# Performance work log

Hardware: AMD Instinct MI355X
Metric: run time of the kernel (lower is better)

## Reference

```python
import jax, jax.numpy as jnp
import numpy as np

G = 16          # spline grid_size
NT = 32         # num_tiles
NS = 2          # num_states
SD = 8          # state_dim
MAXLEN = 2048.0 # max_seq_len
SPREAD = 2.0    # position_spread
LN_EPS = 1e-5


def cubic_bspline(t):
    t = jnp.abs(t)
    r1 = 2.0 / 3.0 - t * t + 0.5 * t ** 3
    r2 = (1.0 / 6.0) * (2.0 - t) ** 3
    return jnp.where(t < 1.0, r1, jnp.where(t < 2.0, r2, jnp.zeros_like(t)))


def ternary(x):
    return jnp.where(x > 0.3, 1.0, jnp.where(x < -0.3, -1.0, 0.0)).astype(x.dtype)


def setup_inputs() -> dict:
    key = jax.random.key(0)
    ks = jax.random.split(key, 14)
    B, T, D = 4, 2048, 1024
    H = D // 4
    x = jax.random.normal(ks[0], (B, T, D), jnp.float32)
    positions = jnp.broadcast_to(jnp.arange(T, dtype=jnp.float32), (B, T))
    states = jax.random.randint(ks[1], (B, T), 0, NS)
    ln_gamma = jnp.ones((D,), jnp.float32)
    ln_beta = jnp.zeros((D,), jnp.float32)
    W1 = jax.random.normal(ks[2], (D, H), jnp.float32) * (1.0 / np.sqrt(D))
    b1 = jnp.zeros((H,), jnp.float32)
    W2 = jax.random.normal(ks[3], (H, 2), jnp.float32) * (1.0 / np.sqrt(H))
    b2 = jnp.zeros((2,), jnp.float32)
    spline_coeffs = jax.random.normal(ks[4], (NT, G, G, 3), jnp.float32) * 0.5
    spline_scales = jnp.ones((NT,), jnp.float32)
    directions = jax.random.normal(ks[5], (NT, D), jnp.float32) * 0.02
    state_signatures = jax.random.normal(ks[6], (NT, SD), jnp.float32) * 0.1
    state_emb = jax.random.normal(ks[7], (NS, SD), jnp.float32)
    state_mod = jnp.ones((NS, NT), jnp.float32)
    output_scale = jnp.ones((1,), jnp.float32) * 0.1
    return dict(x=x, positions=positions, states=states, ln_gamma=ln_gamma,
                ln_beta=ln_beta, W1=W1, b1=b1, W2=W2, b2=b2,
                spline_coeffs=spline_coeffs, spline_scales=spline_scales,
                directions=directions, state_signatures=state_signatures,
                state_emb=state_emb, state_mod=state_mod, output_scale=output_scale)


def reference(x, positions, states, ln_gamma, ln_beta, W1, b1, W2, b2,
              spline_coeffs, spline_scales, directions, state_signatures,
              state_emb, state_mod, output_scale):
    B, T, D = x.shape
    xf = x.reshape(-1, D)                               # [N, D]
    mu = jnp.mean(xf, axis=-1, keepdims=True)
    var = jnp.mean((xf - mu) ** 2, axis=-1, keepdims=True)
    xn = (xf - mu) / jnp.sqrt(var + LN_EPS) * ln_gamma + ln_beta

    # --- three-way routing ---
    sigs = jnp.sign(directions)                         # ternary signatures [NT, D]
    content = xn @ sigs.T                               # [N, NT]
    pos = positions.reshape(-1)
    pn = pos / MAXLEN * NT
    centers = jnp.arange(NT, dtype=xn.dtype)
    spatial = cubic_bspline((pn[:, None] - centers[None, :]) / SPREAD)  # [N, NT]
    st = states.reshape(-1)
    sv = state_emb[st]                                  # [N, SD]
    temporal = jax.nn.sigmoid(sv @ state_signatures.T)  # [N, NT]
    combined = content * spatial * temporal
    probs = jax.nn.softmax(combined * 5.0, axis=-1)
    tile_idx = jnp.argmax(combined, axis=-1)            # [N]
    tile_weights = jnp.take_along_axis(probs, tile_idx[:, None], axis=1)[:, 0]

    # --- compress to 2D spline coordinates ---
    h = jax.nn.gelu(xn @ W1 + b1, approximate=False)
    comp = jnp.tanh(h @ W2 + b2)                        # [N, 2]
    a, b = comp[:, 0], comp[:, 1]

    # --- ternary 2D spline per winning tile (vectorized dispatch) ---
    idx_a = jnp.clip(((a + 1.0) / 2.0 * G).astype(jnp.int32), 0, G - 1)
    idx_b = jnp.clip(((b + 1.0) / 2.0 * G).astype(jnp.int32), 0, G - 1)
    q = spline_coeffs + jax.lax.stop_gradient(ternary(spline_coeffs) - spline_coeffs)
    cell = q[tile_idx, idx_a, idx_b]                    # [N, 3]
    cs = 2.0 / G
    la = (a + 1.0 - idx_a.astype(a.dtype) * cs) / cs
    lb = (b + 1.0 - idx_b.astype(b.dtype) * cs) / cs
    scale = (cell[:, 0] + cell[:, 1] * la + cell[:, 2] * lb) * spline_scales[tile_idx]
    smod = state_mod[st, tile_idx]
    contrib = (scale * smod)[:, None] * directions[tile_idx]  # [N, D]

    out = x + contrib.reshape(B, T, D) * output_scale   # residual, eval (no dropout)
    return out
```

## Files before the change

kernel.cpp:

```cpp
#include <hip/hip_runtime.h>
#include <math.h>

#define NROWS 8192
#define DD    1024
#define HH    256
#define NTT   32
#define NCOLS 288

typedef __attribute__((ext_vector_type(8))) __bf16 bf16x8;
typedef __attribute__((ext_vector_type(4))) float f32x4;

static __device__ __forceinline__ unsigned short f2bf(float f) {
    unsigned int u = __float_as_uint(f);
    unsigned int r = (u + 0x7fffu + ((u >> 16) & 1u)) >> 16;
    return (unsigned short)r;
}

static __device__ __forceinline__ float sgnf(float x) {
    return x > 0.0f ? 1.0f : (x < 0.0f ? -1.0f : 0.0f);
}

static __device__ __forceinline__ float ternf(float x) {
    return x > 0.3f ? 1.0f : (x < -0.3f ? -1.0f : 0.0f);
}

static __device__ __forceinline__ float bspline(float u) {
    float t = fabsf(u);
    if (t < 1.0f) return 0.66666666666666663f - t * t + 0.5f * t * t * t;
    if (t < 2.0f) { float w = 2.0f - t; return 0.16666666666666666f * w * w * w; }
    return 0.0f;
}

__global__ __launch_bounds__(256) void k_prep_ln(const float* __restrict__ W1,
                                                 const float* __restrict__ dirs,
                                                 const float* __restrict__ gamma,
                                                 const float* __restrict__ beta,
                                                 const float* __restrict__ x,
                                                 unsigned short* __restrict__ WT,
                                                 unsigned short* __restrict__ XN) {
    int bid = blockIdx.x;
    int tid = threadIdx.x;
    if (bid < 256) {
        __shared__ float tile[32][33];
        int ktile = bid & 31;
        int ntile = bid >> 5;
        int tx = tid & 31;
        int ty = tid >> 5;
#pragma unroll
        for (int i = 0; i < 4; ++i) {
            int k = ktile * 32 + ty + i * 8;
            int n = ntile * 32 + tx;
            tile[ty + i * 8][tx] = W1[(size_t)k * HH + n];
        }
        __syncthreads();
#pragma unroll
        for (int i = 0; i < 4; ++i) {
            int n = ntile * 32 + ty + i * 8;
            int k = ktile * 32 + tx;
            WT[(size_t)n * DD + k] = f2bf(tile[tx][ty + i * 8]);
        }
    } else if (bid < 288) {
        int r = bid - 256;
        float4 v = ((const float4*)(dirs + (size_t)r * DD))[tid];
        ushort4 o;
        o.x = f2bf(sgnf(v.x)); o.y = f2bf(sgnf(v.y));
        o.z = f2bf(sgnf(v.z)); o.w = f2bf(sgnf(v.w));
        ((ushort4*)(WT + (size_t)(HH + r) * DD))[tid] = o;
    } else {
        int row = bid - 288;
        const float4* xr = (const float4*)(x + (size_t)row * DD);
        float4 v = xr[tid];
        float s  = v.x + v.y + v.z + v.w;
        float sq = v.x * v.x + v.y * v.y + v.z * v.z + v.w * v.w;
#pragma unroll
        for (int off = 32; off; off >>= 1) {
            s  += __shfl_xor(s, off);
            sq += __shfl_xor(sq, off);
        }
        __shared__ float red[8];
        int wid = tid >> 6, lane = tid & 63;
        if (lane == 0) { red[wid] = s; red[wid + 4] = sq; }
        __syncthreads();
        s  = red[0] + red[1] + red[2] + red[3];
        sq = red[4] + red[5] + red[6] + red[7];
        float mu   = s * (1.0f / DD);
        float var  = sq * (1.0f / DD) - mu * mu;
        float rstd = rsqrtf(var + 1e-5f);
        float4 gm = ((const float4*)gamma)[tid];
        float4 bt = ((const float4*)beta)[tid];
        ushort4 o;
        o.x = f2bf((v.x - mu) * rstd * gm.x + bt.x);
        o.y = f2bf((v.y - mu) * rstd * gm.y + bt.y);
        o.z = f2bf((v.z - mu) * rstd * gm.z + bt.z);
        o.w = f2bf((v.w - mu) * rstd * gm.w + bt.w);
        ((ushort4*)(XN + (size_t)row * DD))[tid] = o;
    }
}

__global__ __launch_bounds__(256) void k_gemm(const unsigned short* __restrict__ XN,
                                              const unsigned short* __restrict__ WT,
                                              float* __restrict__ HP) {
    __shared__ short Al[2][32 * 64];
    __shared__ short Bl[2][96 * 64];
    int tid = threadIdx.x;
    int bid = blockIdx.x;
    int swz = (bid & 7) * 96 + (bid >> 3);
    int colblk = swz % 3;
    int rowblk = swz / 3;
    int row0  = rowblk * 32;
    int ncol0 = colblk * 96;
    int lane = tid & 63;
    int wid  = tid >> 6;
    int wm = wid >> 1, wn = wid & 1;
    int l15 = lane & 15, l4 = lane >> 4;

    f32x4 acc[3];
#pragma unroll
    for (int j = 0; j < 3; ++j) acc[j] = (f32x4){0.f, 0.f, 0.f, 0.f};

#define STAGE(kt, buf)                                                           \
    {                                                                            \
                           \
        {                                                                        \
            int r = tid >> 3, g = tid & 7;                                       \
            const unsigned short* srcA =                                         \
                XN + (size_t)(row0 + r) * DD + (kt) * 64 + ((g * 8) ^ ((r & 7) << 3)); \
            __builtin_amdgcn_global_load_lds(                                    \
                (const __attribute__((address_space(1))) void*)(const void*)srcA,\
                (__attribute__((address_space(3))) void*)(void*)(Al[buf] + tid * 8), \
                16, 0, 0);                                                       \
        }                                                                        \
                                            \
        _Pragma("unroll")                                                        \
        for (int ci = 0; ci < 3; ++ci) {                                         \
            int li = ci * 256 + tid;                                             \
            int r  = li >> 3;                                                    \
            int g  = li & 7;                                                     \
            const unsigned short* src =                                          \
                WT + (size_t)(ncol0 + r) * DD + (kt) * 64 + ((g * 8) ^ ((r & 7) << 3)); \
            __builtin_amdgcn_global_load_lds(                                    \
                (const __attribute__((address_space(1))) void*)(const void*)src, \
                (__attribute__((address_space(3))) void*)(void*)(Bl[buf] + li * 8), \
                16, 0, 0);                                                       \
        }                                                                        \
    }

#define COMPUTE(buf)                                                             \
    _Pragma("unroll")                                                            \
    for (int ks = 0; ks < 2; ++ks) {                                             \
        int ra = wm * 16 + l15;                                                  \
        int ca = (ks * 64 + l4 * 16) ^ ((ra & 7) << 4);                          \
        bf16x8 av = *(const bf16x8*)((const char*)Al[buf] + ra * 128 + ca);      \
        bf16x8 bv[3];                                                            \
        _Pragma("unroll")                                                        \
        for (int nf = 0; nf < 3; ++nf) {                                         \
            int rb = wn * 48 + nf * 16 + l15;                                    \
            int cb = (ks * 64 + l4 * 16) ^ ((rb & 7) << 4);                      \
            bv[nf] = *(const bf16x8*)((const char*)Bl[buf] + rb * 128 + cb);     \
        }                                                                        \
        _Pragma("unroll")                                                        \
        for (int nf = 0; nf < 3; ++nf)                                           \
            acc[nf] = __builtin_amdgcn_mfma_f32_16x16x32_bf16(av, bv[nf], acc[nf], 0, 0, 0); \
    }

    STAGE(0, 0);
    __syncthreads();
    for (int kt = 0; kt < 16; ++kt) {
        if (kt < 15) STAGE(kt + 1, (kt + 1) & 1);
        COMPUTE(kt & 1);
        __syncthreads();
    }
#undef STAGE
#undef COMPUTE

#pragma unroll
    for (int nf = 0; nf < 3; ++nf) {
        int colg = ncol0 + wn * 48 + nf * 16 + l15;
        int rl0 = wm * 16 + l4 * 4;
#pragma unroll
        for (int i = 0; i < 4; ++i) {
            HP[(size_t)(row0 + rl0 + i) * NCOLS + colg] = acc[nf][i];
        }
    }
}

__global__ __launch_bounds__(256) void k_epilogue(
    const float* __restrict__ HP, const float* __restrict__ x,
    const float* __restrict__ positions, const int* __restrict__ states,
    const float* __restrict__ b1, const float* __restrict__ W2,
    const float* __restrict__ b2, const float* __restrict__ spc,
    const float* __restrict__ sps, const float* __restrict__ dirs,
    const float* __restrict__ ssig, const float* __restrict__ semb,
    const float* __restrict__ smod, const float* __restrict__ oscale,
    float* __restrict__ out) {
    int wid = threadIdx.x >> 6;
    int lane = threadIdx.x & 63;
    int row = blockIdx.x * 4 + wid;

    const float* hrow = HP + (size_t)row * NCOLS;
    float4 hv  = ((const float4*)hrow)[lane];
    float4 b1v = ((const float4*)b1)[lane];
    float hs[4] = {hv.x, hv.y, hv.z, hv.w};
    float bs[4] = {b1v.x, b1v.y, b1v.z, b1v.w};
    float sa = 0.f, sb = 0.f;
#pragma unroll
    for (int i = 0; i < 4; ++i) {
        float h = hs[i] + bs[i];
        float g = 0.5f * h * (1.0f + erff(h * 0.70710678118654752f));
        int j = lane * 4 + i;
        sa += g * W2[2 * j];
        sb += g * W2[2 * j + 1];
    }
#pragma unroll
    for (int off = 32; off; off >>= 1) {
        sa += __shfl_xor(sa, off);
        sb += __shfl_xor(sb, off);
    }
    float av = tanhf(sa + b2[0]);
    float bv = tanhf(sb + b2[1]);

    int st = states[row];
    float comb;
    if (lane < NTT) {
        float content = hrow[HH + lane];
        float pn = positions[row] * ((float)NTT / 2048.0f);
        float u  = (pn - (float)lane) * 0.5f;
        float spv = bspline(u);
        const float* sg = ssig + lane * 8;
        const float* se = semb + st * 8;
        float d0 = 0.f;
#pragma unroll
        for (int k = 0; k < 8; ++k) d0 += se[k] * sg[k];
        float temporal = 1.0f / (1.0f + expf(-d0));
        comb = content * spv * temporal;
    } else {
        comb = -__builtin_inff();
    }
    int bi = lane;
#pragma unroll
    for (int off = 32; off; off >>= 1) {
        float ov = __shfl_xor(comb, off);
        int   oi = __shfl_xor(bi, off);
        if (ov > comb || (ov == comb && oi < bi)) { comb = ov; bi = oi; }
    }
    int ia = (int)((av + 1.0f) * 8.0f); ia = ia < 0 ? 0 : (ia > 15 ? 15 : ia);
    int ib = (int)((bv + 1.0f) * 8.0f); ib = ib < 0 ? 0 : (ib > 15 ? 15 : ib);
    const float* cc = spc + (((size_t)bi * 16 + ia) * 16 + ib) * 3;
    float c0 = ternf(cc[0]), c1 = ternf(cc[1]), c2 = ternf(cc[2]);
    float la = (av + 1.0f - (float)ia * 0.125f) * 8.0f;
    float lb = (bv + 1.0f - (float)ib * 0.125f) * 8.0f;
    float scale = (c0 + c1 * la + c2 * lb) * sps[bi];
    float sm = smod[st * NTT + bi];
    float cr = scale * sm * oscale[0];

    const float4* xr = (const float4*)(x + (size_t)row * DD);
    const float4* dr = (const float4*)(dirs + (size_t)bi * DD);
    float4* orow = (float4*)(out + (size_t)row * DD);
#pragma unroll
    for (int i = 0; i < 4; ++i) {
        int idx = i * 64 + lane;
        float4 xv = xr[idx];
        float4 dv = dr[idx];
        float4 o;
        o.x = fmaf(cr, dv.x, xv.x);
        o.y = fmaf(cr, dv.y, xv.y);
        o.z = fmaf(cr, dv.z, xv.z);
        o.w = fmaf(cr, dv.w, xv.w);
        orow[idx] = o;
    }
}

extern "C" void kernel_launch(void* const* d_in, const int* in_sizes, int n_in,
                              void* d_out, int out_size, void* d_ws, size_t ws_size,
                              hipStream_t stream) {
    const float* x     = (const float*)d_in[0];
    const float* pos   = (const float*)d_in[1];
    const int*   st    = (const int*)d_in[2];
    const float* gam   = (const float*)d_in[3];
    const float* bet   = (const float*)d_in[4];
    const float* W1    = (const float*)d_in[5];
    const float* b1    = (const float*)d_in[6];
    const float* W2    = (const float*)d_in[7];
    const float* b2    = (const float*)d_in[8];
    const float* spc   = (const float*)d_in[9];
    const float* sps   = (const float*)d_in[10];
    const float* dirs  = (const float*)d_in[11];
    const float* ssig  = (const float*)d_in[12];
    const float* semb  = (const float*)d_in[13];
    const float* smod  = (const float*)d_in[14];
    const float* oscal = (const float*)d_in[15];
    float* out = (float*)d_out;

    char* ws = (char*)d_ws;
    unsigned short* WT = (unsigned short*)ws;
    unsigned short* XN = (unsigned short*)(ws + 1048576);
    float* HP          = (float*)(ws + 1048576 + 16777216);

    k_prep_ln<<<288 + NROWS, 256, 0, stream>>>(W1, dirs, gam, bet, x, WT, XN);
    k_gemm<<<768, 256, 0, stream>>>(XN, WT, HP);
    k_epilogue<<<NROWS / 4, 256, 0, stream>>>(HP, x, pos, st, b1, W2, b2, spc, sps,
                                              dirs, ssig, semb, smod, oscal, out);
}
```

Measured before the change: 48.02 us.

## Fuse GEMM and epilogue into one kernel with full-width column tiles in LDS

The GEMM and epilogue kernels are merged. Each 576-thread block of 9 waves now computes all 288 output columns for 32 rows, stages the result in shared memory, and runs the routing/spline epilogue directly from LDS. This removes the HP global round-trip and one kernel launch. The temporal sigmoid is also precomputed per state instead of per row. In exchange only 256 blocks are launched, each needing a large LDS footprint (about 111KB) and re-streaming the whole weight matrix. That lowers occupancy and parallelism and may hurt the GEMM phase.

```diff
diff --git a/kernel.cpp b/kernel.cpp
--- a/kernel.cpp
+++ b/kernel.cpp
@@ -6,6 +6,7 @@
 #define HH    256
 #define NTT   32
 #define NCOLS 288
+#define HPS   296
 
 typedef __attribute__((ext_vector_type(8))) __bf16 bf16x8;
 typedef __attribute__((ext_vector_type(4))) float f32x4;
@@ -97,31 +98,36 @@
     }
 }
 
-__global__ __launch_bounds__(256) void k_gemm(const unsigned short* __restrict__ XN,
-                                              const unsigned short* __restrict__ WT,
-                                              float* __restrict__ HP) {
+__global__ __launch_bounds__(576) void k_fused(
+    const unsigned short* __restrict__ XN, const unsigned short* __restrict__ WT,
+    const float* __restrict__ x,
+    const float* __restrict__ positions, const int* __restrict__ states,
+    const float* __restrict__ b1, const float* __restrict__ W2,
+    const float* __restrict__ b2, const float* __restrict__ spc,
+    const float* __restrict__ sps, const float* __restrict__ dirs,
+    const float* __restrict__ ssig, const float* __restrict__ semb,
+    const float* __restrict__ smod, const float* __restrict__ oscale,
+    float* __restrict__ out) {
     __shared__ short Al[2][32 * 64];
-    __shared__ short Bl[2][96 * 64];
-    int tid = threadIdx.x;
-    int bid = blockIdx.x;
-    int swz = (bid & 7) * 96 + (bid >> 3);
-    int colblk = swz % 3;
-    int rowblk = swz / 3;
-    int row0  = rowblk * 32;
-    int ncol0 = colblk * 96;
+    __shared__ short Bl[2][NCOLS * 64];
+    __shared__ float HPl[32 * HPS];
+
+    int tid  = threadIdx.x;
+    int row0 = blockIdx.x * 32;
     int lane = tid & 63;
     int wid  = tid >> 6;
-    int wm = wid >> 1, wn = wid & 1;
     int l15 = lane & 15, l4 = lane >> 4;
 
-    f32x4 acc[3];
-#pragma unroll
-    for (int j = 0; j < 3; ++j) acc[j] = (f32x4){0.f, 0.f, 0.f, 0.f};
+    f32x4 acc[2][2];
+#pragma unroll
+    for (int i = 0; i < 2; ++i)
+#pragma unroll
+        for (int j = 0; j < 2; ++j) acc[i][j] = (f32x4){0.f, 0.f, 0.f, 0.f};
 
 #define STAGE(kt, buf)                                                           \
     {                                                                            \
-                           \
-        {                                                                        \
+             \
+        if (tid < 256) {                                                         \
             int r = tid >> 3, g = tid & 7;                                       \
             const unsigned short* srcA =                                         \
                 XN + (size_t)(row0 + r) * DD + (kt) * 64 + ((g * 8) ^ ((r & 7) << 3)); \
@@ -130,14 +136,14 @@
                 (__attribute__((address_space(3))) void*)(void*)(Al[buf] + tid * 8), \
                 16, 0, 0);                                                       \
         }                                                                        \
-                                            \
+                 \
         _Pragma("unroll")                                                        \
-        for (int ci = 0; ci < 3; ++ci) {                                         \
-            int li = ci * 256 + tid;                                             \
+        for (int ci = 0; ci < 4; ++ci) {                                         \
+            int li = ci * 576 + tid;                                             \
             int r  = li >> 3;                                                    \
             int g  = li & 7;                                                     \
             const unsigned short* src =                                          \
-                WT + (size_t)(ncol0 + r) * DD + (kt) * 64 + ((g * 8) ^ ((r & 7) << 3)); \
+                WT + (size_t)r * DD + (kt) * 64 + ((g * 8) ^ ((r & 7) << 3));    \
             __builtin_amdgcn_global_load_lds(                                    \
                 (const __attribute__((address_space(1))) void*)(const void*)src, \
                 (__attribute__((address_space(3))) void*)(void*)(Bl[buf] + li * 8), \
@@ -148,19 +154,25 @@
 #define COMPUTE(buf)                                                             \
     _Pragma("unroll")                                                            \
     for (int ks = 0; ks < 2; ++ks) {                                             \
-        int ra = wm * 16 + l15;                                                  \
-        int ca = (ks * 64 + l4 * 16) ^ ((ra & 7) << 4);                          \
-        bf16x8 av = *(const bf16x8*)((const char*)Al[buf] + ra * 128 + ca);      \
-        bf16x8 bv[3];                                                            \
+        bf16x8 av[2], bv[2];                                                     \
         _Pragma("unroll")                                                        \
-        for (int nf = 0; nf < 3; ++nf) {                                         \
-            int rb = wn * 48 + nf * 16 + l15;                                    \
+        for (int mf = 0; mf < 2; ++mf) {                                         \
+            int ra = mf * 16 + l15;                                              \
+            int ca = (ks * 64 + l4 * 16) ^ ((ra & 7) << 4);                      \
+            av[mf] = *(const bf16x8*)((const char*)Al[buf] + ra * 128 + ca);     \
+        }                                                                        \
+        _Pragma("unroll")                                                        \
+        for (int nf = 0; nf < 2; ++nf) {                                         \
+            int rb = wid * 32 + nf * 16 + l15;                                   \
             int cb = (ks * 64 + l4 * 16) ^ ((rb & 7) << 4);                      \
             bv[nf] = *(const bf16x8*)((const char*)Bl[buf] + rb * 128 + cb);     \
         }                                                                        \
         _Pragma("unroll")                                                        \
-        for (int nf = 0; nf < 3; ++nf)                                           \
-            acc[nf] = __builtin_amdgcn_mfma_f32_16x16x32_bf16(av, bv[nf], acc[nf], 0, 0, 0); \
+        for (int mf = 0; mf < 2; ++mf)                                           \
+            _Pragma("unroll")                                                    \
+            for (int nf = 0; nf < 2; ++nf)                                       \
+                acc[mf][nf] = __builtin_amdgcn_mfma_f32_16x16x32_bf16(           \
+                    av[mf], bv[nf], acc[mf][nf], 0, 0, 0);                       \
     }
 
     STAGE(0, 0);
@@ -174,99 +186,102 @@
 #undef COMPUTE
 
 #pragma unroll
-    for (int nf = 0; nf < 3; ++nf) {
-        int colg = ncol0 + wn * 48 + nf * 16 + l15;
-        int rl0 = wm * 16 + l4 * 4;
+    for (int mf = 0; mf < 2; ++mf) {
+#pragma unroll
+        for (int nf = 0; nf < 2; ++nf) {
+            int colg = wid * 32 + nf * 16 + l15;
+            int r0 = mf * 16 + l4 * 4;
+#pragma unroll
+            for (int i = 0; i < 4; ++i) {
+                HPl[(r0 + i) * HPS + colg] = acc[mf][nf][i];
+            }
+        }
+    }
+    __syncthreads();
+
+    float4 b1v = ((const float4*)b1)[lane];
+    float w2a[4], w2b[4];
+#pragma unroll
+    for (int i = 0; i < 4; ++i) {
+        int j = lane * 4 + i;
+        w2a[i] = W2[2 * j];
+        w2b[i] = W2[2 * j + 1];
+    }
+    float tvs[2] = {0.f, 0.f};
+    if (lane < NTT) {
+#pragma unroll
+        for (int s2 = 0; s2 < 2; ++s2) {
+            float d0 = 0.f;
+#pragma unroll
+            for (int k = 0; k < 8; ++k) d0 += semb[s2 * 8 + k] * ssig[lane * 8 + k];
+            tvs[s2] = 1.0f / (1.0f + expf(-d0));
+        }
+    }
+    float osc = oscale[0];
+    float bb0 = b2[0], bb1 = b2[1];
+
+    for (int r = wid; r < 32; r += 9) {
+        int row = row0 + r;
+        float4 hv = *(const float4*)&HPl[r * HPS + lane * 4];
+        float hs[4] = {hv.x, hv.y, hv.z, hv.w};
+        float bs[4] = {b1v.x, b1v.y, b1v.z, b1v.w};
+        float sa = 0.f, sb2 = 0.f;
 #pragma unroll
         for (int i = 0; i < 4; ++i) {
-            HP[(size_t)(row0 + rl0 + i) * NCOLS + colg] = acc[nf][i];
-        }
-    }
-}
-
-__global__ __launch_bounds__(256) void k_epilogue(
-    const float* __restrict__ HP, const float* __restrict__ x,
-    const float* __restrict__ positions, const int* __restrict__ states,
-    const float* __restrict__ b1, const float* __restrict__ W2,
-    const float* __restrict__ b2, const float* __restrict__ spc,
-    const float* __restrict__ sps, const float* __restrict__ dirs,
-    const float* __restrict__ ssig, const float* __restrict__ semb,
-    const float* __restrict__ smod, const float* __restrict__ oscale,
-    float* __restrict__ out) {
-    int wid = threadIdx.x >> 6;
-    int lane = threadIdx.x & 63;
-    int row = blockIdx.x * 4 + wid;
-
-    const float* hrow = HP + (size_t)row * NCOLS;
-    float4 hv  = ((const float4*)hrow)[lane];
-    float4 b1v = ((const float4*)b1)[lane];
-    float hs[4] = {hv.x, hv.y, hv.z, hv.w};
-    float bs[4] = {b1v.x, b1v.y, b1v.z, b1v.w};
-    float sa = 0.f, sb = 0.f;
-#pragma unroll
-    for (int i = 0; i < 4; ++i) {
-        float h = hs[i] + bs[i];
-        float g = 0.5f * h * (1.0f + erff(h * 0.70710678118654752f));
-        int j = lane * 4 + i;
-        sa += g * W2[2 * j];
-        sb += g * W2[2 * j + 1];
-    }
-#pragma unroll
-    for (int off = 32; off; off >>= 1) {
-        sa += __shfl_xor(sa, off);
-        sb += __shfl_xor(sb, off);
-    }
-    float av = tanhf(sa + b2[0]);
-    float bv = tanhf(sb + b2[1]);
-
-    int st = states[row];
-    float comb;
-    if (lane < NTT) {
-        float content = hrow[HH + lane];
-        float pn = positions[row] * ((float)NTT / 2048.0f);
-        float u  = (pn - (float)lane) * 0.5f;
-        float spv = bspline(u);
-        const float* sg = ssig + lane * 8;
-        const float* se = semb + st * 8;
-        float d0 = 0.f;
-#pragma unroll
-        for (int k = 0; k < 8; ++k) d0 += se[k] * sg[k];
-        float temporal = 1.0f / (1.0f + expf(-d0));
-        comb = content * spv * temporal;
-    } else {
-        comb = -__builtin_inff();
-    }
-    int bi = lane;
-#pragma unroll
-    for (int off = 32; off; off >>= 1) {
-        float ov = __shfl_xor(comb, off);
-        int   oi = __shfl_xor(bi, off);
-        if (ov > comb || (ov == comb && oi < bi)) { comb = ov; bi = oi; }
-    }
-    int ia = (int)((av + 1.0f) * 8.0f); ia = ia < 0 ? 0 : (ia > 15 ? 15 : ia);
-    int ib = (int)((bv + 1.0f) * 8.0f); ib = ib < 0 ? 0 : (ib > 15 ? 15 : ib);
-    const float* cc = spc + (((size_t)bi * 16 + ia) * 16 + ib) * 3;
-    float c0 = ternf(cc[0]), c1 = ternf(cc[1]), c2 = ternf(cc[2]);
-    float la = (av + 1.0f - (float)ia * 0.125f) * 8.0f;
-    float lb = (bv + 1.0f - (float)ib * 0.125f) * 8.0f;
-    float scale = (c0 + c1 * la + c2 * lb) * sps[bi];
-    float sm = smod[st * NTT + bi];
-    float cr = scale * sm * oscale[0];
-
-    const float4* xr = (const float4*)(x + (size_t)row * DD);
-    const float4* dr = (const float4*)(dirs + (size_t)bi * DD);
-    float4* orow = (float4*)(out + (size_t)row * DD);
-#pragma unroll
-    for (int i = 0; i < 4; ++i) {
-        int idx = i * 64 + lane;
-        float4 xv = xr[idx];
-        float4 dv = dr[idx];
-        float4 o;
-        o.x = fmaf(cr, dv.x, xv.x);
-        o.y = fmaf(cr, dv.y, xv.y);
-        o.z = fmaf(cr, dv.z, xv.z);
-        o.w = fmaf(cr, dv.w, xv.w);
-        orow[idx] = o;
+            float h = hs[i] + bs[i];
+            float g = 0.5f * h * (1.0f + erff(h * 0.70710678118654752f));
+            sa  += g * w2a[i];
+            sb2 += g * w2b[i];
+        }
+#pragma unroll
+        for (int off = 32; off; off >>= 1) {
+            sa  += __shfl_xor(sa, off);
+            sb2 += __shfl_xor(sb2, off);
+        }
+        float av2 = tanhf(sa + bb0);
+        float bv2 = tanhf(sb2 + bb1);
+
+        int st = states[row];
+        float comb;
+        if (lane < NTT) {
+            float content = HPl[r * HPS + HH + lane];
+            float pn = positions[row] * ((float)NTT / 2048.0f);
+            float spv = bspline((pn - (float)lane) * 0.5f);
+            comb = content * spv * tvs[st];
+        } else {
+            comb = -__builtin_inff();
+        }
+        int bi = lane;
+#pragma unroll
+        for (int off = 32; off; off >>= 1) {
+            float ov = __shfl_xor(comb, off);
+            int   oi = __shfl_xor(bi, off);
+            if (ov > comb || (ov == comb && oi < bi)) { comb = ov; bi = oi; }
+        }
+        int ia = (int)((av2 + 1.0f) * 8.0f); ia = ia < 0 ? 0 : (ia > 15 ? 15 : ia);
+        int ib = (int)((bv2 + 1.0f) * 8.0f); ib = ib < 0 ? 0 : (ib > 15 ? 15 : ib);
+        const float* cc = spc + (((size_t)bi * 16 + ia) * 16 + ib) * 3;
+        float c0 = ternf(cc[0]), c1 = ternf(cc[1]), c2 = ternf(cc[2]);
+        float la = (av2 + 1.0f - (float)ia * 0.125f) * 8.0f;
+        float lb = (bv2 + 1.0f - (float)ib * 0.125f) * 8.0f;
+        float scale = (c0 + c1 * la + c2 * lb) * sps[bi];
+        float cr = scale * smod[st * NTT + bi] * osc;
+
+        const float4* xr = (const float4*)(x + (size_t)row * DD);
+        const float4* dr = (const float4*)(dirs + (size_t)bi * DD);
+        float4* orow = (float4*)(out + (size_t)row * DD);
+#pragma unroll
+        for (int i = 0; i < 4; ++i) {
+            int idx = i * 64 + lane;
+            float4 xv = xr[idx];
+            float4 dv = dr[idx];
+            float4 o;
+            o.x = fmaf(cr, dv.x, xv.x);
+            o.y = fmaf(cr, dv.y, xv.y);
+            o.z = fmaf(cr, dv.z, xv.z);
+            o.w = fmaf(cr, dv.w, xv.w);
+            orow[idx] = o;
+        }
     }
 }
 
@@ -294,10 +309,8 @@
     char* ws = (char*)d_ws;
     unsigned short* WT = (unsigned short*)ws;
     unsigned short* XN = (unsigned short*)(ws + 1048576);
-    float* HP          = (float*)(ws + 1048576 + 16777216);
 
     k_prep_ln<<<288 + NROWS, 256, 0, stream>>>(W1, dirs, gam, bet, x, WT, XN);
-    k_gemm<<<768, 256, 0, stream>>>(XN, WT, HP);
-    k_epilogue<<<NROWS / 4, 256, 0, stream>>>(HP, x, pos, st, b1, W2, b2, spc, sps,
-                                              dirs, ssig, semb, smod, oscal, out);
-}
+    k_fused<<<NROWS / 32, 576, 0, stream>>>(XN, WT, x, pos, st, b1, W2, b2,
+                                            spc, sps, dirs, ssig, semb, smod, oscal, out);
+}
```

After: 44.16 us. 8.0% less time.
